# Kernel tuning notes

Hardware: AMD Instinct MI355X
Metric: run time of the kernel (lower is better)

## Reference

```python
import jax, jax.numpy as jnp
import numpy as np

N, M, D_K, D_V = 8192, 8192, 128, 128
SCALING = 1.0 / D_K  # module uses 1/d_k, NOT 1/sqrt(d_k)


def setup_inputs() -> dict:
    key = jax.random.key(0)
    kq, kk, kv = jax.random.split(key, 3)
    Q = jax.random.normal(kq, (N, D_K), dtype=jnp.float32)
    K = jax.random.normal(kk, (M, D_K), dtype=jnp.float32)
    V = jax.random.normal(kv, (M, D_V), dtype=jnp.float32)
    return {"Q": Q, "K": K, "V": V}


def reference(Q, K, V):
    # dots = Q @ K^T * (1/d_k)  -> [N, M]
    dots = jnp.einsum("nd,md->nm", Q, K) * SCALING
    # softmax over keys; dropout p=0 is identity
    attn = jax.nn.softmax(dots, axis=-1)
    # output = attn @ V -> [N, d_v]
    return jnp.einsum("nm,mv->nv", attn, V)
```

## Files before the change

kernel.cpp:

```cpp
#include <hip/hip_runtime.h>
#include <hip/hip_bf16.h>
#include <cstdint>
#include <cstddef>


typedef __attribute__((ext_vector_type(8))) short short8;
typedef __attribute__((ext_vector_type(4))) short shortx4;
typedef __attribute__((ext_vector_type(4))) float floatx4;
typedef __attribute__((ext_vector_type(16))) float floatx16;
typedef __attribute__((ext_vector_type(8))) _Float16 half8;

#define N_Q    8192
#define N_KV   8192
#define DHEAD  128
#define NSPLIT 8
#define BK     64
#define QSCALE (1.4426950408889634f / 128.0f)

static __device__ __forceinline__ unsigned short f2bf(float x) {
  __hip_bfloat16 h = __float2bfloat16(x);
  unsigned short u;
  __builtin_memcpy(&u, &h, 2);
  return u;
}

static __device__ __forceinline__ uint32_t cvt_pk_bf16(float lo, float hi) {
  uint32_t r;
  asm("v_cvt_pk_bf16_f32 %0, %1, %2" : "=v"(r) : "v"(lo), "v"(hi));
  return r;
}

#define MFMA32(a, b, c) __builtin_amdgcn_mfma_f32_32x32x16_bf16((a), (b), (c), 0, 0, 0)

#define GLD_LDS16(g, l)                                                        \
  __builtin_amdgcn_global_load_lds(                                            \
      (const __attribute__((address_space(1))) void*)(g),                      \
      (__attribute__((address_space(3))) void*)(l), 16, 0, 0)

__global__ void cvt_kernel(const float* __restrict__ K,
                           const float* __restrict__ V,
                           unsigned short* __restrict__ Kbc,
                           unsigned short* __restrict__ Vtc) {
  int bid = blockIdx.x;
  if (bid < 512) {
    int tid = bid * 256 + threadIdx.x;
    int ki = tid & 63;
    int ch = (tid >> 6) & 15;
    int b  = tid >> 10;
    const float* src = K + ((size_t)(b * 64 + ki) * DHEAD + ch * 8);
    floatx4 f0 = *(const floatx4*)src;
    floatx4 f1 = *(const floatx4*)(src + 4);
    short8 o;
    o[0] = (short)f2bf(f0[0]); o[1] = (short)f2bf(f0[1]);
    o[2] = (short)f2bf(f0[2]); o[3] = (short)f2bf(f0[3]);
    o[4] = (short)f2bf(f1[0]); o[5] = (short)f2bf(f1[1]);
    o[6] = (short)f2bf(f1[2]); o[7] = (short)f2bf(f1[3]);
    *(short8*)(Kbc + (size_t)tid * 8) = o;
  } else {
    int tid = (bid - 512) * 256 + threadIdx.x;
    int kh = tid & 1;
    int dv = (tid >> 1) & 127;
    int c2 = (tid >> 8) & 7;
    int b  = tid >> 11;
    int k0 = b * 64 + c2 * 8 + kh * 4;
    shortx4 o;
    o[0] = (short)f2bf(V[(size_t)(k0 + 0) * DHEAD + dv]);
    o[1] = (short)f2bf(V[(size_t)(k0 + 1) * DHEAD + dv]);
    o[2] = (short)f2bf(V[(size_t)(k0 + 2) * DHEAD + dv]);
    o[3] = (short)f2bf(V[(size_t)(k0 + 3) * DHEAD + dv]);
    *(shortx4*)(Vtc + (size_t)tid * 4) = o;
  }
}

__global__ __launch_bounds__(256, 2) void attn_kernel(
    const float* __restrict__ Q, const unsigned short* __restrict__ Kbc,
    const unsigned short* __restrict__ Vtc, _Float16* __restrict__ Opart,
    float* __restrict__ Lst) {
  __shared__ unsigned short lds[2 * 16384];

  const int t = threadIdx.x;
  const int w = t >> 6;
  const int lane = t & 63;
  const int h = lane >> 5;
  const int c = lane & 31;
  const int qbase = blockIdx.x * 128 + w * 32;
  const int sp = blockIdx.y;

  short8 qf[8];
  {
    const float* qrow = Q + (size_t)(qbase + c) * DHEAD + h * 8;
#pragma unroll
    for (int dc = 0; dc < 8; ++dc) {
      floatx4 f0 = *(const floatx4*)(qrow + dc * 16);
      floatx4 f1 = *(const floatx4*)(qrow + dc * 16 + 4);
      short8 s;
      s[0] = (short)f2bf(f0[0] * QSCALE); s[1] = (short)f2bf(f0[1] * QSCALE);
      s[2] = (short)f2bf(f0[2] * QSCALE); s[3] = (short)f2bf(f0[3] * QSCALE);
      s[4] = (short)f2bf(f1[0] * QSCALE); s[5] = (short)f2bf(f1[1] * QSCALE);
      s[6] = (short)f2bf(f1[2] * QSCALE); s[7] = (short)f2bf(f1[3] * QSCALE);
      qf[dc] = s;
    }
  }

  floatx16 acc[4];
#pragma unroll
  for (int i = 0; i < 4; ++i)
#pragma unroll
    for (int r = 0; r < 16; ++r) acc[i][r] = 0.f;
  float lsum = 0.f;

  const int NT = N_KV / NSPLIT / BK;
  const int kb0 = sp * NT;

  auto stage = [&](unsigned short* dstK, int kb) {
    const unsigned short* kg = Kbc + (size_t)kb * 8192;
    const unsigned short* vg = Vtc + (size_t)kb * 8192;
#pragma unroll
    for (int i = 0; i < 4; ++i) {
      int slab = w * 4 + i;
      GLD_LDS16(kg + slab * 512 + lane * 8, dstK + slab * 512);
      GLD_LDS16(vg + slab * 512 + lane * 8, dstK + 8192 + slab * 512);
    }
  };

  stage(lds, kb0);
  __syncthreads();

  for (int it = 0; it < NT; ++it) {
    const int cur = it & 1;
    if (it + 1 < NT) stage(lds + (cur ^ 1) * 16384, kb0 + it + 1);

    const short8* KsF  = (const short8*)(lds + cur * 16384);
    const short8* VtsF = (const short8*)(lds + cur * 16384 + 8192);

#pragma unroll
    for (int st = 0; st < 2; ++st) {
      floatx16 sc;
#pragma unroll
      for (int r = 0; r < 16; ++r) sc[r] = 0.f;
      __builtin_amdgcn_s_setprio(1);
#pragma unroll
      for (int dc = 0; dc < 8; ++dc) {
        short8 a = KsF[(dc * 2 + h) * 64 + st * 32 + c];
        sc = MFMA32(a, qf[dc], sc);
      }
      __builtin_amdgcn_s_setprio(0);

      float p[16];
#pragma unroll
      for (int r = 0; r < 16; ++r) p[r] = __builtin_amdgcn_exp2f(sc[r]);
      lsum += ((((p[0] + p[1]) + (p[2] + p[3])) +
                ((p[4] + p[5]) + (p[6] + p[7]))) +
               (((p[8] + p[9]) + (p[10] + p[11])) +
                ((p[12] + p[13]) + (p[14] + p[15]))));

#pragma unroll
      for (int kc2 = 0; kc2 < 2; ++kc2) {
        const int g = kc2 * 8;
        uint32_t x0 = cvt_pk_bf16(p[g + 0], p[g + 1]);
        uint32_t x1 = cvt_pk_bf16(p[g + 2], p[g + 3]);
        uint32_t y0 = cvt_pk_bf16(p[g + 4], p[g + 5]);
        uint32_t y1 = cvt_pk_bf16(p[g + 6], p[g + 7]);
        auto s0 = __builtin_amdgcn_permlane32_swap(x0, y0, false, false);
        auto s1 = __builtin_amdgcn_permlane32_swap(x1, y1, false, false);
        union { uint32_t u[4]; short8 s; } pu;
        pu.u[0] = s0[0];
        pu.u[1] = s1[0];
        pu.u[2] = s0[1];
        pu.u[3] = s1[1];
        const int kc = st * 2 + kc2;
        __builtin_amdgcn_s_setprio(1);
#pragma unroll
        for (int nb = 0; nb < 4; ++nb) {
          short8 bv = VtsF[(kc * 2 + h) * 128 + nb * 32 + c];
          acc[nb] = MFMA32(pu.s, bv, acc[nb]);
        }
        __builtin_amdgcn_s_setprio(0);
      }
    }
    __syncthreads();
  }

  lsum += __shfl_xor(lsum, 32, 64);
  if (h == 0) Lst[(size_t)sp * N_Q + qbase + c] = lsum;
  _Float16* op = Opart + ((size_t)sp * N_Q + qbase) * DHEAD;
#pragma unroll
  for (int nb = 0; nb < 4; ++nb)
#pragma unroll
    for (int r = 0; r < 16; ++r) {
      int row = (r & 3) + 8 * (r >> 2) + 4 * h;
      op[(size_t)row * DHEAD + nb * 32 + c] = (_Float16)acc[nb][r];
    }
}

__global__ void merge_kernel(const _Float16* __restrict__ Opart,
                             const float* __restrict__ Lst,
                             float* __restrict__ out) {
  int tid = blockIdx.x * blockDim.x + threadIdx.x;
  int g = tid >> 4;
  int d0 = (tid & 15) * 8;
  float den = 0.f;
  float num[8] = {0.f, 0.f, 0.f, 0.f, 0.f, 0.f, 0.f, 0.f};
#pragma unroll
  for (int s = 0; s < NSPLIT; ++s) {
    den += Lst[(size_t)s * N_Q + g];
    half8 o = *(const half8*)(Opart + ((size_t)s * N_Q + g) * DHEAD + d0);
#pragma unroll
    for (int j = 0; j < 8; ++j) num[j] += (float)o[j];
  }
  float inv = 1.0f / den;
  floatx4 r0 = (floatx4){num[0] * inv, num[1] * inv, num[2] * inv, num[3] * inv};
  floatx4 r1 = (floatx4){num[4] * inv, num[5] * inv, num[6] * inv, num[7] * inv};
  float* dst = out + (size_t)g * DHEAD + d0;
  *(floatx4*)dst = r0;
  *(floatx4*)(dst + 4) = r1;
}

extern "C" void kernel_launch(void* const* d_in, const int* in_sizes, int n_in,
                              void* d_out, int out_size, void* d_ws,
                              size_t ws_size, hipStream_t stream) {
  const float* Q = (const float*)d_in[0];
  const float* K = (const float*)d_in[1];
  const float* V = (const float*)d_in[2];
  float* out = (float*)d_out;

  char* ws = (char*)d_ws;
  unsigned short* Kbc = (unsigned short*)(ws);
  unsigned short* Vtc = (unsigned short*)(ws + (2u << 20));
  _Float16* Opart = (_Float16*)(ws + (4u << 20));
  float* Lst = (float*)(ws + (20u << 20));

  cvt_kernel<<<dim3(1536), dim3(256), 0, stream>>>(K, V, Kbc, Vtc);
  attn_kernel<<<dim3(N_Q / 128, NSPLIT), dim3(256), 0, stream>>>(Q, Kbc, Vtc,
                                                                 Opart, Lst);
  merge_kernel<<<dim3(512), dim3(256), 0, stream>>>(Opart, Lst, out);
}
```

Measured before the change: 106.0 us.

## Process two 32-row query blocks per wave and double the KV split count

Each wave now handles 64 query rows as two 32-row sub-blocks. K and V fragments are read from LDS once and fed to MFMAs for both sub-blocks, which halves LDS traffic per MFMA. To keep enough blocks in the grid, the KV split count goes from 8 to 16, and the workspace offset for the partial sums moves to fit the larger partial output. The cost is roughly double the accumulator registers, which may hurt occupancy under launch_bounds(256,2), plus more partial-output traffic for the merge kernel.

```diff
diff --git a/kernel.cpp b/kernel.cpp
--- a/kernel.cpp
+++ b/kernel.cpp
@@ -13,7 +13,7 @@
 #define N_Q    8192
 #define N_KV   8192
 #define DHEAD  128
-#define NSPLIT 8
+#define NSPLIT 16
 #define BK     64
 #define QSCALE (1.4426950408889634f / 128.0f)
 
@@ -83,12 +83,13 @@
   const int lane = t & 63;
   const int h = lane >> 5;
   const int c = lane & 31;
-  const int qbase = blockIdx.x * 128 + w * 32;
+  const int qbase = blockIdx.x * 256 + w * 64;
   const int sp = blockIdx.y;
 
-  short8 qf[8];
-  {
-    const float* qrow = Q + (size_t)(qbase + c) * DHEAD + h * 8;
+  short8 qf[2][8];
+#pragma unroll
+  for (int qb = 0; qb < 2; ++qb) {
+    const float* qrow = Q + (size_t)(qbase + qb * 32 + c) * DHEAD + h * 8;
 #pragma unroll
     for (int dc = 0; dc < 8; ++dc) {
       floatx4 f0 = *(const floatx4*)(qrow + dc * 16);
@@ -98,16 +99,18 @@
       s[2] = (short)f2bf(f0[2] * QSCALE); s[3] = (short)f2bf(f0[3] * QSCALE);
       s[4] = (short)f2bf(f1[0] * QSCALE); s[5] = (short)f2bf(f1[1] * QSCALE);
       s[6] = (short)f2bf(f1[2] * QSCALE); s[7] = (short)f2bf(f1[3] * QSCALE);
-      qf[dc] = s;
+      qf[qb][dc] = s;
     }
   }
 
-  floatx16 acc[4];
-#pragma unroll
-  for (int i = 0; i < 4; ++i)
-#pragma unroll
-    for (int r = 0; r < 16; ++r) acc[i][r] = 0.f;
-  float lsum = 0.f;
+  floatx16 acc[2][4];
+#pragma unroll
+  for (int qb = 0; qb < 2; ++qb)
+#pragma unroll
+    for (int i = 0; i < 4; ++i)
+#pragma unroll
+      for (int r = 0; r < 16; ++r) acc[qb][i][r] = 0.f;
+  float lsum[2] = {0.f, 0.f};
 
   const int NT = N_KV / NSPLIT / BK;
   const int kb0 = sp * NT;
@@ -123,6 +126,18 @@
     }
   };
 
+  auto packfrag = [&](const float* p, int g) -> short8 {
+    uint32_t x0 = cvt_pk_bf16(p[g + 0], p[g + 1]);
+    uint32_t x1 = cvt_pk_bf16(p[g + 2], p[g + 3]);
+    uint32_t y0 = cvt_pk_bf16(p[g + 4], p[g + 5]);
+    uint32_t y1 = cvt_pk_bf16(p[g + 6], p[g + 7]);
+    auto s0 = __builtin_amdgcn_permlane32_swap(x0, y0, false, false);
+    auto s1 = __builtin_amdgcn_permlane32_swap(x1, y1, false, false);
+    union { uint32_t u[4]; short8 s; } pu;
+    pu.u[0] = s0[0]; pu.u[1] = s1[0]; pu.u[2] = s0[1]; pu.u[3] = s1[1];
+    return pu.s;
+  };
+
   stage(lds, kb0);
   __syncthreads();
 
@@ -135,62 +150,67 @@
 
 #pragma unroll
     for (int st = 0; st < 2; ++st) {
-      floatx16 sc;
-#pragma unroll
-      for (int r = 0; r < 16; ++r) sc[r] = 0.f;
+      short8 ka[8];
+#pragma unroll
+      for (int dc = 0; dc < 8; ++dc)
+        ka[dc] = KsF[(dc * 2 + h) * 64 + st * 32 + c];
+
+      floatx16 sc[2];
+#pragma unroll
+      for (int qb = 0; qb < 2; ++qb)
+#pragma unroll
+        for (int r = 0; r < 16; ++r) sc[qb][r] = 0.f;
       __builtin_amdgcn_s_setprio(1);
 #pragma unroll
       for (int dc = 0; dc < 8; ++dc) {
-        short8 a = KsF[(dc * 2 + h) * 64 + st * 32 + c];
-        sc = MFMA32(a, qf[dc], sc);
+        sc[0] = MFMA32(ka[dc], qf[0][dc], sc[0]);
+        sc[1] = MFMA32(ka[dc], qf[1][dc], sc[1]);
       }
       __builtin_amdgcn_s_setprio(0);
 
-      float p[16];
-#pragma unroll
-      for (int r = 0; r < 16; ++r) p[r] = __builtin_amdgcn_exp2f(sc[r]);
-      lsum += ((((p[0] + p[1]) + (p[2] + p[3])) +
-                ((p[4] + p[5]) + (p[6] + p[7]))) +
-               (((p[8] + p[9]) + (p[10] + p[11])) +
-                ((p[12] + p[13]) + (p[14] + p[15]))));
-
+      short8 pa[2][2];
+#pragma unroll
+      for (int qb = 0; qb < 2; ++qb) {
+        float p[16];
+#pragma unroll
+        for (int r = 0; r < 16; ++r) p[r] = __builtin_amdgcn_exp2f(sc[qb][r]);
+        lsum[qb] += ((((p[0] + p[1]) + (p[2] + p[3])) +
+                      ((p[4] + p[5]) + (p[6] + p[7]))) +
+                     (((p[8] + p[9]) + (p[10] + p[11])) +
+                      ((p[12] + p[13]) + (p[14] + p[15]))));
+        pa[qb][0] = packfrag(p, 0);
+        pa[qb][1] = packfrag(p, 8);
+      }
+
+      __builtin_amdgcn_s_setprio(1);
 #pragma unroll
       for (int kc2 = 0; kc2 < 2; ++kc2) {
-        const int g = kc2 * 8;
-        uint32_t x0 = cvt_pk_bf16(p[g + 0], p[g + 1]);
-        uint32_t x1 = cvt_pk_bf16(p[g + 2], p[g + 3]);
-        uint32_t y0 = cvt_pk_bf16(p[g + 4], p[g + 5]);
-        uint32_t y1 = cvt_pk_bf16(p[g + 6], p[g + 7]);
-        auto s0 = __builtin_amdgcn_permlane32_swap(x0, y0, false, false);
-        auto s1 = __builtin_amdgcn_permlane32_swap(x1, y1, false, false);
-        union { uint32_t u[4]; short8 s; } pu;
-        pu.u[0] = s0[0];
-        pu.u[1] = s1[0];
-        pu.u[2] = s0[1];
-        pu.u[3] = s1[1];
         const int kc = st * 2 + kc2;
-        __builtin_amdgcn_s_setprio(1);
 #pragma unroll
         for (int nb = 0; nb < 4; ++nb) {
           short8 bv = VtsF[(kc * 2 + h) * 128 + nb * 32 + c];
-          acc[nb] = MFMA32(pu.s, bv, acc[nb]);
+          acc[0][nb] = MFMA32(pa[0][kc2], bv, acc[0][nb]);
+          acc[1][nb] = MFMA32(pa[1][kc2], bv, acc[1][nb]);
         }
-        __builtin_amdgcn_s_setprio(0);
-      }
+      }
+      __builtin_amdgcn_s_setprio(0);
     }
     __syncthreads();
   }
 
-  lsum += __shfl_xor(lsum, 32, 64);
-  if (h == 0) Lst[(size_t)sp * N_Q + qbase + c] = lsum;
-  _Float16* op = Opart + ((size_t)sp * N_Q + qbase) * DHEAD;
-#pragma unroll
-  for (int nb = 0; nb < 4; ++nb)
-#pragma unroll
-    for (int r = 0; r < 16; ++r) {
-      int row = (r & 3) + 8 * (r >> 2) + 4 * h;
-      op[(size_t)row * DHEAD + nb * 32 + c] = (_Float16)acc[nb][r];
-    }
+#pragma unroll
+  for (int qb = 0; qb < 2; ++qb) {
+    float l = lsum[qb] + __shfl_xor(lsum[qb], 32, 64);
+    if (h == 0) Lst[(size_t)sp * N_Q + qbase + qb * 32 + c] = l;
+    _Float16* op = Opart + ((size_t)sp * N_Q + qbase + qb * 32) * DHEAD;
+#pragma unroll
+    for (int nb = 0; nb < 4; ++nb)
+#pragma unroll
+      for (int r = 0; r < 16; ++r) {
+        int row = (r & 3) + 8 * (r >> 2) + 4 * h;
+        op[(size_t)row * DHEAD + nb * 32 + c] = (_Float16)acc[qb][nb][r];
+      }
+  }
 }
 
 __global__ void merge_kernel(const _Float16* __restrict__ Opart,
@@ -228,10 +248,10 @@
   unsigned short* Kbc = (unsigned short*)(ws);
   unsigned short* Vtc = (unsigned short*)(ws + (2u << 20));
   _Float16* Opart = (_Float16*)(ws + (4u << 20));
-  float* Lst = (float*)(ws + (20u << 20));
+  float* Lst = (float*)(ws + (36u << 20));
 
   cvt_kernel<<<dim3(1536), dim3(256), 0, stream>>>(K, V, Kbc, Vtc);
-  attn_kernel<<<dim3(N_Q / 128, NSPLIT), dim3(256), 0, stream>>>(Q, Kbc, Vtc,
+  attn_kernel<<<dim3(N_Q / 256, NSPLIT), dim3(256), 0, stream>>>(Q, Kbc, Vtc,
                                                                  Opart, Lst);
   merge_kernel<<<dim3(512), dim3(256), 0, stream>>>(Opart, Lst, out);
 }
```

Result: slower. 132.6 us (+25.1%).

## Double KV splits, halve KV tile, raise occupancy to four blocks per CU

Applied to the files above, without the earlier changes.

Changes the split-K schedule from 8 to 16 KV splits with a 32-key tile instead of 64, halving LDS per block and asking the compiler for 4 blocks per CU. The K/V conversion layouts, staging, and inner loop are reworked for the smaller tile, and the partial output workspace grows accordingly. The aim is more resident waves to hide latency and a fuller grid. In exchange the merge pass reads twice as many fp16 partials, each tile iteration does half as much work per barrier, and the tighter register budget risks spills.

```diff
diff --git a/kernel.cpp b/kernel.cpp
--- a/kernel.cpp
+++ b/kernel.cpp
@@ -13,8 +13,8 @@
 #define N_Q    8192
 #define N_KV   8192
 #define DHEAD  128
-#define NSPLIT 8
-#define BK     64
+#define NSPLIT 16
+#define BK     32
 #define QSCALE (1.4426950408889634f / 128.0f)
 
 static __device__ __forceinline__ unsigned short f2bf(float x) {
@@ -44,10 +44,10 @@
   int bid = blockIdx.x;
   if (bid < 512) {
     int tid = bid * 256 + threadIdx.x;
-    int ki = tid & 63;
-    int ch = (tid >> 6) & 15;
-    int b  = tid >> 10;
-    const float* src = K + ((size_t)(b * 64 + ki) * DHEAD + ch * 8);
+    int ki  = tid & 31;
+    int ch  = (tid >> 5) & 15;
+    int b32 = tid >> 9;
+    const float* src = K + ((size_t)(b32 * 32 + ki) * DHEAD + ch * 8);
     floatx4 f0 = *(const floatx4*)src;
     floatx4 f1 = *(const floatx4*)(src + 4);
     short8 o;
@@ -58,11 +58,11 @@
     *(short8*)(Kbc + (size_t)tid * 8) = o;
   } else {
     int tid = (bid - 512) * 256 + threadIdx.x;
-    int kh = tid & 1;
-    int dv = (tid >> 1) & 127;
-    int c2 = (tid >> 8) & 7;
-    int b  = tid >> 11;
-    int k0 = b * 64 + c2 * 8 + kh * 4;
+    int kh  = tid & 1;
+    int dv  = (tid >> 1) & 127;
+    int c2  = (tid >> 8) & 3;
+    int b32 = tid >> 10;
+    int k0 = b32 * 32 + c2 * 8 + kh * 4;
     shortx4 o;
     o[0] = (short)f2bf(V[(size_t)(k0 + 0) * DHEAD + dv]);
     o[1] = (short)f2bf(V[(size_t)(k0 + 1) * DHEAD + dv]);
@@ -72,11 +72,11 @@
   }
 }
 
-__global__ __launch_bounds__(256, 2) void attn_kernel(
+__global__ __launch_bounds__(256, 4) void attn_kernel(
     const float* __restrict__ Q, const unsigned short* __restrict__ Kbc,
     const unsigned short* __restrict__ Vtc, _Float16* __restrict__ Opart,
     float* __restrict__ Lst) {
-  __shared__ unsigned short lds[2 * 16384];
+  __shared__ unsigned short lds[2 * 8192];
 
   const int t = threadIdx.x;
   const int w = t >> 6;
@@ -113,14 +113,35 @@
   const int kb0 = sp * NT;
 
   auto stage = [&](unsigned short* dstK, int kb) {
-    const unsigned short* kg = Kbc + (size_t)kb * 8192;
-    const unsigned short* vg = Vtc + (size_t)kb * 8192;
-#pragma unroll
-    for (int i = 0; i < 4; ++i) {
-      int slab = w * 4 + i;
+    const unsigned short* kg = Kbc + (size_t)kb * 4096;
+    const unsigned short* vg = Vtc + (size_t)kb * 4096;
+#pragma unroll
+    for (int i = 0; i < 2; ++i) {
+      int slab = w * 2 + i;
       GLD_LDS16(kg + slab * 512 + lane * 8, dstK + slab * 512);
-      GLD_LDS16(vg + slab * 512 + lane * 8, dstK + 8192 + slab * 512);
-    }
+      GLD_LDS16(vg + slab * 512 + lane * 8, dstK + 4096 + slab * 512);
+    }
+  };
+
+  auto pack8 = [&](const floatx16& sc, int g, float& ls) -> short8 {
+    float p0 = __builtin_amdgcn_exp2f(sc[g + 0]);
+    float p1 = __builtin_amdgcn_exp2f(sc[g + 1]);
+    float p2 = __builtin_amdgcn_exp2f(sc[g + 2]);
+    float p3 = __builtin_amdgcn_exp2f(sc[g + 3]);
+    float p4 = __builtin_amdgcn_exp2f(sc[g + 4]);
+    float p5 = __builtin_amdgcn_exp2f(sc[g + 5]);
+    float p6 = __builtin_amdgcn_exp2f(sc[g + 6]);
+    float p7 = __builtin_amdgcn_exp2f(sc[g + 7]);
+    ls += ((p0 + p1) + (p2 + p3)) + ((p4 + p5) + (p6 + p7));
+    uint32_t x0 = cvt_pk_bf16(p0, p1);
+    uint32_t x1 = cvt_pk_bf16(p2, p3);
+    uint32_t y0 = cvt_pk_bf16(p4, p5);
+    uint32_t y1 = cvt_pk_bf16(p6, p7);
+    auto s0 = __builtin_amdgcn_permlane32_swap(x0, y0, false, false);
+    auto s1 = __builtin_amdgcn_permlane32_swap(x1, y1, false, false);
+    union { uint32_t u[4]; short8 s; } pu;
+    pu.u[0] = s0[0]; pu.u[1] = s1[0]; pu.u[2] = s0[1]; pu.u[3] = s1[1];
+    return pu.s;
   };
 
   stage(lds, kb0);
@@ -128,56 +149,37 @@
 
   for (int it = 0; it < NT; ++it) {
     const int cur = it & 1;
-    if (it + 1 < NT) stage(lds + (cur ^ 1) * 16384, kb0 + it + 1);
-
-    const short8* KsF  = (const short8*)(lds + cur * 16384);
-    const short8* VtsF = (const short8*)(lds + cur * 16384 + 8192);
-
-#pragma unroll
-    for (int st = 0; st < 2; ++st) {
-      floatx16 sc;
-#pragma unroll
-      for (int r = 0; r < 16; ++r) sc[r] = 0.f;
-      __builtin_amdgcn_s_setprio(1);
-#pragma unroll
-      for (int dc = 0; dc < 8; ++dc) {
-        short8 a = KsF[(dc * 2 + h) * 64 + st * 32 + c];
-        sc = MFMA32(a, qf[dc], sc);
+    if (it + 1 < NT) stage(lds + (cur ^ 1) * 8192, kb0 + it + 1);
+
+    const short8* KsF  = (const short8*)(lds + cur * 8192);
+    const short8* VtsF = (const short8*)(lds + cur * 8192 + 4096);
+
+    floatx16 sc;
+#pragma unroll
+    for (int r = 0; r < 16; ++r) sc[r] = 0.f;
+    __builtin_amdgcn_s_setprio(1);
+#pragma unroll
+    for (int dc = 0; dc < 8; ++dc) {
+      short8 ka = KsF[(dc * 2 + h) * 32 + c];
+      sc = MFMA32(ka, qf[dc], sc);
+    }
+    __builtin_amdgcn_s_setprio(0);
+
+    short8 pa0 = pack8(sc, 0, lsum);
+    short8 pa1 = pack8(sc, 8, lsum);
+
+    __builtin_amdgcn_s_setprio(1);
+#pragma unroll
+    for (int kc = 0; kc < 2; ++kc) {
+      const short8 a = kc ? pa1 : pa0;
+#pragma unroll
+      for (int nb = 0; nb < 4; ++nb) {
+        short8 bv = VtsF[(kc * 2 + h) * 128 + nb * 32 + c];
+        acc[nb] = MFMA32(a, bv, acc[nb]);
       }
-      __builtin_amdgcn_s_setprio(0);
-
-      float p[16];
-#pragma unroll
-      for (int r = 0; r < 16; ++r) p[r] = __builtin_amdgcn_exp2f(sc[r]);
-      lsum += ((((p[0] + p[1]) + (p[2] + p[3])) +
-                ((p[4] + p[5]) + (p[6] + p[7]))) +
-               (((p[8] + p[9]) + (p[10] + p[11])) +
-                ((p[12] + p[13]) + (p[14] + p[15]))));
-
-#pragma unroll
-      for (int kc2 = 0; kc2 < 2; ++kc2) {
-        const int g = kc2 * 8;
-        uint32_t x0 = cvt_pk_bf16(p[g + 0], p[g + 1]);
-        uint32_t x1 = cvt_pk_bf16(p[g + 2], p[g + 3]);
-        uint32_t y0 = cvt_pk_bf16(p[g + 4], p[g + 5]);
-        uint32_t y1 = cvt_pk_bf16(p[g + 6], p[g + 7]);
-        auto s0 = __builtin_amdgcn_permlane32_swap(x0, y0, false, false);
-        auto s1 = __builtin_amdgcn_permlane32_swap(x1, y1, false, false);
-        union { uint32_t u[4]; short8 s; } pu;
-        pu.u[0] = s0[0];
-        pu.u[1] = s1[0];
-        pu.u[2] = s0[1];
-        pu.u[3] = s1[1];
-        const int kc = st * 2 + kc2;
-        __builtin_amdgcn_s_setprio(1);
-#pragma unroll
-        for (int nb = 0; nb < 4; ++nb) {
-          short8 bv = VtsF[(kc * 2 + h) * 128 + nb * 32 + c];
-          acc[nb] = MFMA32(pu.s, bv, acc[nb]);
-        }
-        __builtin_amdgcn_s_setprio(0);
-      }
-    }
+    }
+    __builtin_amdgcn_s_setprio(0);
+
     __syncthreads();
   }
 
@@ -228,7 +230,7 @@
   unsigned short* Kbc = (unsigned short*)(ws);
   unsigned short* Vtc = (unsigned short*)(ws + (2u << 20));
   _Float16* Opart = (_Float16*)(ws + (4u << 20));
-  float* Lst = (float*)(ws + (20u << 20));
+  float* Lst = (float*)(ws + (36u << 20));
 
   cvt_kernel<<<dim3(1536), dim3(256), 0, stream>>>(K, V, Kbc, Vtc);
   attn_kernel<<<dim3(N_Q / 128, NSPLIT), dim3(256), 0, stream>>>(Q, Kbc, Vtc,
```

Result: slower. 114.4 us (+7.9%).

## Overlap LDS prefetch with explicit vmcnt waits and split QK MFMA chains

Applied to the files above, without the earlier changes.

Replaces the __syncthreads after each tile with explicit s_waitcnt vmcnt plus s_barrier, so the next tile's global-to-LDS loads stay in flight while the current tile is computed. The QK^T MFMA accumulation is split into two independent even/odd chains that are summed afterwards, which shortens the dependency chain. The exp/pack work is hoisted ahead of the PV MFMAs and the priority toggles are merged. The hand-coded vmcnt count depends on the number of loads issued per stage, which is fragile if the staging changes. Dropping the initial sync also relies on the first loop iteration's wait and barrier for correctness.

```diff
diff --git a/kernel.cpp b/kernel.cpp
--- a/kernel.cpp
+++ b/kernel.cpp
@@ -123,62 +123,77 @@
     }
   };
 
+  auto pack8 = [&](const floatx16& sc, int g, float& ls) -> short8 {
+    float p0 = __builtin_amdgcn_exp2f(sc[g + 0]);
+    float p1 = __builtin_amdgcn_exp2f(sc[g + 1]);
+    float p2 = __builtin_amdgcn_exp2f(sc[g + 2]);
+    float p3 = __builtin_amdgcn_exp2f(sc[g + 3]);
+    float p4 = __builtin_amdgcn_exp2f(sc[g + 4]);
+    float p5 = __builtin_amdgcn_exp2f(sc[g + 5]);
+    float p6 = __builtin_amdgcn_exp2f(sc[g + 6]);
+    float p7 = __builtin_amdgcn_exp2f(sc[g + 7]);
+    ls += ((p0 + p1) + (p2 + p3)) + ((p4 + p5) + (p6 + p7));
+    uint32_t x0 = cvt_pk_bf16(p0, p1);
+    uint32_t x1 = cvt_pk_bf16(p2, p3);
+    uint32_t y0 = cvt_pk_bf16(p4, p5);
+    uint32_t y1 = cvt_pk_bf16(p6, p7);
+    auto s0 = __builtin_amdgcn_permlane32_swap(x0, y0, false, false);
+    auto s1 = __builtin_amdgcn_permlane32_swap(x1, y1, false, false);
+    union { uint32_t u[4]; short8 s; } pu;
+    pu.u[0] = s0[0]; pu.u[1] = s1[0]; pu.u[2] = s0[1]; pu.u[3] = s1[1];
+    return pu.s;
+  };
+
   stage(lds, kb0);
-  __syncthreads();
 
   for (int it = 0; it < NT; ++it) {
     const int cur = it & 1;
-    if (it + 1 < NT) stage(lds + (cur ^ 1) * 16384, kb0 + it + 1);
+    if (it + 1 < NT) {
+      stage(lds + (cur ^ 1) * 16384, kb0 + it + 1);
+      asm volatile("s_waitcnt vmcnt(8)" ::: "memory");
+    } else {
+      asm volatile("s_waitcnt vmcnt(0)" ::: "memory");
+    }
+    __builtin_amdgcn_s_barrier();
 
     const short8* KsF  = (const short8*)(lds + cur * 16384);
     const short8* VtsF = (const short8*)(lds + cur * 16384 + 8192);
 
 #pragma unroll
     for (int st = 0; st < 2; ++st) {
-      floatx16 sc;
-#pragma unroll
-      for (int r = 0; r < 16; ++r) sc[r] = 0.f;
+      floatx16 scE, scO;
+#pragma unroll
+      for (int r = 0; r < 16; ++r) { scE[r] = 0.f; scO[r] = 0.f; }
       __builtin_amdgcn_s_setprio(1);
 #pragma unroll
-      for (int dc = 0; dc < 8; ++dc) {
-        short8 a = KsF[(dc * 2 + h) * 64 + st * 32 + c];
-        sc = MFMA32(a, qf[dc], sc);
+      for (int j = 0; j < 4; ++j) {
+        short8 kaE = KsF[((2 * j) * 2 + h) * 64 + st * 32 + c];
+        short8 kaO = KsF[((2 * j + 1) * 2 + h) * 64 + st * 32 + c];
+        scE = MFMA32(kaE, qf[2 * j], scE);
+        scO = MFMA32(kaO, qf[2 * j + 1], scO);
       }
       __builtin_amdgcn_s_setprio(0);
-
-      float p[16];
-#pragma unroll
-      for (int r = 0; r < 16; ++r) p[r] = __builtin_amdgcn_exp2f(sc[r]);
-      lsum += ((((p[0] + p[1]) + (p[2] + p[3])) +
-                ((p[4] + p[5]) + (p[6] + p[7]))) +
-               (((p[8] + p[9]) + (p[10] + p[11])) +
-                ((p[12] + p[13]) + (p[14] + p[15]))));
-
+      floatx16 sc;
+#pragma unroll
+      for (int r = 0; r < 16; ++r) sc[r] = scE[r] + scO[r];
+
+      short8 pa0 = pack8(sc, 0, lsum);
+      short8 pa1 = pack8(sc, 8, lsum);
+
+      __builtin_amdgcn_s_setprio(1);
 #pragma unroll
       for (int kc2 = 0; kc2 < 2; ++kc2) {
-        const int g = kc2 * 8;
-        uint32_t x0 = cvt_pk_bf16(p[g + 0], p[g + 1]);
-        uint32_t x1 = cvt_pk_bf16(p[g + 2], p[g + 3]);
-        uint32_t y0 = cvt_pk_bf16(p[g + 4], p[g + 5]);
-        uint32_t y1 = cvt_pk_bf16(p[g + 6], p[g + 7]);
-        auto s0 = __builtin_amdgcn_permlane32_swap(x0, y0, false, false);
-        auto s1 = __builtin_amdgcn_permlane32_swap(x1, y1, false, false);
-        union { uint32_t u[4]; short8 s; } pu;
-        pu.u[0] = s0[0];
-        pu.u[1] = s1[0];
-        pu.u[2] = s0[1];
-        pu.u[3] = s1[1];
         const int kc = st * 2 + kc2;
-        __builtin_amdgcn_s_setprio(1);
+        const short8 a = kc2 ? pa1 : pa0;
 #pragma unroll
         for (int nb = 0; nb < 4; ++nb) {
           short8 bv = VtsF[(kc * 2 + h) * 128 + nb * 32 + c];
-          acc[nb] = MFMA32(pu.s, bv, acc[nb]);
+          acc[nb] = MFMA32(a, bv, acc[nb]);
         }
-        __builtin_amdgcn_s_setprio(0);
       }
-    }
-    __syncthreads();
+      __builtin_amdgcn_s_setprio(0);
+    }
+    __builtin_amdgcn_s_barrier();
   }
 
   lsum += __shfl_xor(lsum, 32, 64);
```

Measured after the change: 108.3 us. +2.1%, slower.
